# Performance work log

Hardware: AMD Instinct MI355X
Metric: run time of the kernel (lower is better)

The kernel has to match this reference:

```python
import jax, jax.numpy as jnp
import numpy as np

B, N, C, H, D = 1, 4096, 256, 8, 64  # batch, seq, channels, heads, head_dim


def setup_inputs() -> dict:
    key = jax.random.key(0)
    ks = jax.random.split(key, 11)
    s = 0.02
    return {
        "q_x": jax.random.normal(ks[0], (B, N, C), jnp.float32),
        "k_x": jax.random.normal(ks[1], (B, N, C), jnp.float32),
        "v_x": jax.random.normal(ks[2], (B, N, C), jnp.float32),
        "bias": jax.random.normal(ks[3], (B, 1, N, N), jnp.float32),
        "wq": jax.random.normal(ks[4], (H * D, C), jnp.float32) * s,
        "wk": jax.random.normal(ks[5], (H * D, C), jnp.float32) * s,
        "wv": jax.random.normal(ks[6], (H * D, C), jnp.float32) * s,
        "wg": jax.random.normal(ks[7], (H * D, C), jnp.float32) * s,
        "bg": jnp.ones((H * D,), jnp.float32),  # gating bias init = 1
        "wo": jax.random.normal(ks[8], (C, H * D), jnp.float32) * s,
        "bo": jnp.zeros((C,), jnp.float32),
        "q_chunk_size": 256,
        "kv_chunk_size": 1024,
    }


def reference(q_x, k_x, v_x, bias, wq, wk, wv, wg, bg, wo, bo,
              q_chunk_size, kv_chunk_size):
    # The chunked Rabe-Staats loop computes exact softmax attention; the
    # chunk sizes are memory knobs only, so the reference computes the
    # mathematically identical full attention.
    q = (q_x @ wq.T).reshape(*q_x.shape[:-1], H, D) / jnp.sqrt(jnp.asarray(D, q_x.dtype))
    k = (k_x @ wk.T).reshape(*k_x.shape[:-1], H, D)
    v = (v_x @ wv.T).reshape(*v_x.shape[:-1], H, D)
    logits = jnp.einsum("bqhd,bkhd->bhqk", q, k) + bias  # [B,H,Q,K]
    p = jax.nn.softmax(logits, axis=-1)
    o = jnp.einsum("bkhd,bhqk->bqhd", v, p)  # [B,Q,H,D]
    g = jax.nn.sigmoid(q_x @ wg.T + bg).reshape(*q_x.shape[:-1], H, D)
    o = o * g
    o = o.reshape(*o.shape[:-2], H * D)
    return o @ wo.T + bo
```

## Files before the change

### kernel.cpp

```cpp
#include <hip/hip_runtime.h>
#include <stdint.h>

#define NN 4096
#define CC 256
#define HD 512
#define DD 64
#define KSPLIT 2
#define KCHUNK (NN / KSPLIT)

typedef __attribute__((ext_vector_type(8))) short short8;
typedef __attribute__((ext_vector_type(4))) float floatx4;

__device__ __forceinline__ unsigned short f2bf(float x) {
    union { float f; unsigned int u; } v; v.f = x;
    unsigned int u = v.u + 0x7fffu + ((v.u >> 16) & 1u);
    return (unsigned short)(u >> 16);
}
__device__ __forceinline__ float bf2f(unsigned short s) {
    union { unsigned int u; float f; } v; v.u = ((unsigned int)s) << 16;
    return v.f;
}

__global__ __launch_bounds__(256) void proj_kernel(
    const float* __restrict__ qx, const float* __restrict__ kx,
    const float* __restrict__ vx,
    const float* __restrict__ wq, const float* __restrict__ wk,
    const float* __restrict__ wv, const float* __restrict__ wg,
    const float* __restrict__ bg,
    unsigned short* __restrict__ Qb, unsigned short* __restrict__ Kb,
    unsigned short* __restrict__ VbT, unsigned short* __restrict__ Gb)
{
    const int mode = blockIdx.z;
    const float* X = (mode == 1) ? kx : (mode == 2) ? vx : qx;
    const float* W = (mode == 0) ? wq : (mode == 1) ? wk : (mode == 2) ? wv : wg;

    const int m0 = blockIdx.x * 64;
    const int n0 = blockIdx.y * 64;
    const int tid = threadIdx.x;
    const int wid = tid >> 6;
    const int lane = tid & 63;
    const int quad = lane >> 4;
    const int ln = lane & 15;

    __shared__ __align__(16) unsigned short Xs[64 * 72];
    __shared__ __align__(16) unsigned short Ws[64 * 72];

    floatx4 acc[4] = {};

    for (int k0 = 0; k0 < CC; k0 += 64) {
        #pragma unroll
        for (int i = 0; i < 4; i++) {
            int idx = i * 256 + tid;
            int r = idx >> 4, c4 = idx & 15;
            float4 x4 = *(const float4*)&X[(size_t)(m0 + r) * CC + k0 + c4 * 4];
            ushort4 p;
            p.x = f2bf(x4.x); p.y = f2bf(x4.y); p.z = f2bf(x4.z); p.w = f2bf(x4.w);
            *(ushort4*)&Xs[r * 72 + c4 * 4] = p;
        }
        #pragma unroll
        for (int i = 0; i < 4; i++) {
            int idx = i * 256 + tid;
            int r = idx >> 4, c4 = idx & 15;
            float4 w4 = *(const float4*)&W[(size_t)(n0 + r) * CC + k0 + c4 * 4];
            ushort4 p;
            p.x = f2bf(w4.x); p.y = f2bf(w4.y); p.z = f2bf(w4.z); p.w = f2bf(w4.w);
            *(ushort4*)&Ws[r * 72 + c4 * 4] = p;
        }
        __syncthreads();

        #pragma unroll
        for (int ks = 0; ks < 64; ks += 32) {
            short8 a = *(const short8*)&Xs[(wid * 16 + ln) * 72 + ks + quad * 8];
            #pragma unroll
            for (int n = 0; n < 4; n++) {
                short8 b = *(const short8*)&Ws[(n * 16 + ln) * 72 + ks + quad * 8];
                acc[n] = __builtin_amdgcn_mfma_f32_16x16x32_bf16(a, b, acc[n], 0, 0, 0);
            }
        }
        __syncthreads();
    }

    if (mode == 2) {
        #pragma unroll
        for (int n = 0; n < 4; n++) {
            int cl = n * 16 + ln;
            #pragma unroll
            for (int r = 0; r < 4; r++) {
                int rl = wid * 16 + quad * 4 + r;
                Xs[cl * 72 + rl] = f2bf(acc[n][r]);
            }
        }
        __syncthreads();
        #pragma unroll
        for (int i = 0; i < 2; i++) {
            int idx = i * 256 + tid;
            int d = idx >> 3, m8 = idx & 7;
            short8 vv = *(const short8*)&Xs[d * 72 + m8 * 8];
            *(short8*)&VbT[(size_t)(n0 + d) * NN + m0 + m8 * 8] = vv;
        }
    } else {
        unsigned short* Out = (mode == 0) ? Qb : (mode == 1) ? Kb : Gb;
        #pragma unroll
        for (int n = 0; n < 4; n++) {
            int col = n0 + n * 16 + ln;
            float bgv = (mode == 3) ? bg[col] : 0.0f;
            #pragma unroll
            for (int r = 0; r < 4; r++) {
                int row = m0 + wid * 16 + quad * 4 + r;
                float v = acc[n][r];
                if (mode == 0)      v *= 0.125f;
                else if (mode == 3) v = 1.0f / (1.0f + __expf(-(v + bgv)));
                Out[(size_t)row * HD + col] = f2bf(v);
            }
        }
    }
}

__global__ __launch_bounds__(256) void attn_kernel(
    const unsigned short* __restrict__ Qb, const unsigned short* __restrict__ Kb,
    const unsigned short* __restrict__ VbT,
    const float* __restrict__ bias,
    float* __restrict__ Opart, float* __restrict__ Lpart)
{
    const int h = blockIdx.y;
    const int q0 = blockIdx.x * 64;
    const int sp = blockIdx.z;
    const int kbeg = sp * KCHUNK;
    const int tid = threadIdx.x;
    const int wid = tid >> 6;
    const int lane = tid & 63;
    const int quad = lane >> 4;
    const int ln = lane & 15;

    __shared__ __align__(16) unsigned short Qs[64 * 72];
    __shared__ __align__(16) unsigned short Ks[64 * 72];
    __shared__ __align__(16) unsigned short Vs[64 * 72];
    __shared__ __align__(16) unsigned short Ps[64 * 72];

    #pragma unroll
    for (int i = 0; i < 2; i++) {
        int idx = i * 256 + tid;
        int r = idx >> 3, c8 = idx & 7;
        short8 qv = *(const short8*)&Qb[(size_t)(q0 + r) * HD + h * DD + c8 * 8];
        *(short8*)&Qs[r * 72 + c8 * 8] = qv;
    }

    floatx4 O[4] = {};
    float lsum[4] = {0.0f, 0.0f, 0.0f, 0.0f};

    for (int k0 = kbeg; k0 < kbeg + KCHUNK; k0 += 64) {
        #pragma unroll
        for (int i = 0; i < 2; i++) {
            int idx = i * 256 + tid;
            int r = idx >> 3, c8 = idx & 7;
            short8 kv = *(const short8*)&Kb[(size_t)(k0 + r) * HD + h * DD + c8 * 8];
            *(short8*)&Ks[r * 72 + c8 * 8] = kv;
        }
        #pragma unroll
        for (int i = 0; i < 2; i++) {
            int idx = i * 256 + tid;
            int d = idx >> 3, c8 = idx & 7;
            short8 vv = *(const short8*)&VbT[(size_t)(h * DD + d) * NN + k0 + c8 * 8];
            *(short8*)&Vs[d * 72 + c8 * 8] = vv;
        }

        float bv[4][4];
        #pragma unroll
        for (int r = 0; r < 4; r++) {
            int grow = q0 + wid * 16 + quad * 4 + r;
            const float* brow = &bias[(size_t)grow * NN + k0];
            #pragma unroll
            for (int n = 0; n < 4; n++) bv[r][n] = brow[n * 16 + ln];
        }
        __syncthreads();

        floatx4 S[4] = {};
        #pragma unroll
        for (int ks = 0; ks < 64; ks += 32) {
            short8 a = *(const short8*)&Qs[(wid * 16 + ln) * 72 + ks + quad * 8];
            #pragma unroll
            for (int n = 0; n < 4; n++) {
                short8 b = *(const short8*)&Ks[(n * 16 + ln) * 72 + ks + quad * 8];
                S[n] = __builtin_amdgcn_mfma_f32_16x16x32_bf16(a, b, S[n], 0, 0, 0);
            }
        }

        #pragma unroll
        for (int r = 0; r < 4; r++) {
            #pragma unroll
            for (int n = 0; n < 4; n++) {
                float p = __expf(S[n][r] + bv[r][n]);
                lsum[r] += p;
                Ps[(wid * 16 + quad * 4 + r) * 72 + n * 16 + ln] = f2bf(p);
            }
        }

        #pragma unroll
        for (int ks = 0; ks < 64; ks += 32) {
            short8 a = *(const short8*)&Ps[(wid * 16 + ln) * 72 + ks + quad * 8];
            #pragma unroll
            for (int nd = 0; nd < 4; nd++) {
                short8 b = *(const short8*)&Vs[(nd * 16 + ln) * 72 + ks + quad * 8];
                O[nd] = __builtin_amdgcn_mfma_f32_16x16x32_bf16(a, b, O[nd], 0, 0, 0);
            }
        }
        __syncthreads();
    }

    #pragma unroll
    for (int r = 0; r < 4; r++) {
        #pragma unroll
        for (int off = 1; off < 16; off <<= 1)
            lsum[r] += __shfl_xor(lsum[r], off);
        int grow = q0 + wid * 16 + quad * 4 + r;
        size_t base = ((size_t)(sp * 8 + h) * NN + grow) * 64;
        #pragma unroll
        for (int nd = 0; nd < 4; nd++)
            Opart[base + nd * 16 + ln] = O[nd][r];
        if (ln == 0)
            Lpart[(size_t)(sp * 8 + h) * NN + grow] = lsum[r];
    }
}

__global__ __launch_bounds__(256) void combine_kernel(
    const float* __restrict__ Opart, const float* __restrict__ Lpart,
    const unsigned short* __restrict__ Gb, unsigned short* __restrict__ OGb)
{
    const int tid = threadIdx.x;
    const int d = tid & 63;
    const int flat = blockIdx.x * 4 + (tid >> 6);
    const int h = flat >> 12;
    const int q = flat & (NN - 1);

    float l0 = Lpart[(size_t)(0 * 8 + h) * NN + q];
    float l1 = Lpart[(size_t)(1 * 8 + h) * NN + q];
    float inv = 1.0f / (l0 + l1);

    size_t o0 = ((size_t)(0 * 8 + h) * NN + q) * 64 + d;
    size_t o1 = ((size_t)(1 * 8 + h) * NN + q) * 64 + d;
    float o = (Opart[o0] + Opart[o1]) * inv;

    int col = h * DD + d;
    float g = bf2f(Gb[(size_t)q * HD + col]);
    OGb[(size_t)q * HD + col] = f2bf(o * g);
}

__global__ __launch_bounds__(256) void outproj_kernel(
    const unsigned short* __restrict__ OGb, const float* __restrict__ wo,
    const float* __restrict__ bo, float* __restrict__ out)
{
    const int m0 = blockIdx.x * 64;
    const int n0 = blockIdx.y * 64;
    const int tid = threadIdx.x;
    const int wid = tid >> 6;
    const int lane = tid & 63;
    const int quad = lane >> 4;
    const int ln = lane & 15;

    __shared__ __align__(16) unsigned short Xs[64 * 72];
    __shared__ __align__(16) unsigned short Ws[64 * 72];

    floatx4 acc[4] = {};

    for (int k0 = 0; k0 < HD; k0 += 64) {
        #pragma unroll
        for (int i = 0; i < 2; i++) {
            int idx = i * 256 + tid;
            int r = idx >> 3, c8 = idx & 7;
            *(short8*)&Xs[r * 72 + c8 * 8] =
                *(const short8*)&OGb[(size_t)(m0 + r) * HD + k0 + c8 * 8];
        }
        #pragma unroll
        for (int i = 0; i < 4; i++) {
            int idx = i * 256 + tid;
            int r = idx >> 4, c4 = idx & 15;
            float4 w4 = *(const float4*)&wo[(size_t)(n0 + r) * HD + k0 + c4 * 4];
            ushort4 p;
            p.x = f2bf(w4.x); p.y = f2bf(w4.y); p.z = f2bf(w4.z); p.w = f2bf(w4.w);
            *(ushort4*)&Ws[r * 72 + c4 * 4] = p;
        }
        __syncthreads();

        #pragma unroll
        for (int ks = 0; ks < 64; ks += 32) {
            short8 a = *(const short8*)&Xs[(wid * 16 + ln) * 72 + ks + quad * 8];
            #pragma unroll
            for (int n = 0; n < 4; n++) {
                short8 b = *(const short8*)&Ws[(n * 16 + ln) * 72 + ks + quad * 8];
                acc[n] = __builtin_amdgcn_mfma_f32_16x16x32_bf16(a, b, acc[n], 0, 0, 0);
            }
        }
        __syncthreads();
    }

    #pragma unroll
    for (int n = 0; n < 4; n++) {
        int col = n0 + n * 16 + ln;
        float bov = bo[col];
        #pragma unroll
        for (int r = 0; r < 4; r++) {
            int row = m0 + wid * 16 + quad * 4 + r;
            out[(size_t)row * CC + col] = acc[n][r] + bov;
        }
    }
}

extern "C" void kernel_launch(void* const* d_in, const int* in_sizes, int n_in,
                              void* d_out, int out_size, void* d_ws, size_t ws_size,
                              hipStream_t stream) {
    const float* qx   = (const float*)d_in[0];
    const float* kx   = (const float*)d_in[1];
    const float* vx   = (const float*)d_in[2];
    const float* bias = (const float*)d_in[3];
    const float* wq   = (const float*)d_in[4];
    const float* wk   = (const float*)d_in[5];
    const float* wv   = (const float*)d_in[6];
    const float* wg   = (const float*)d_in[7];
    const float* bg   = (const float*)d_in[8];
    const float* wo   = (const float*)d_in[9];
    const float* bo   = (const float*)d_in[10];
    float* out = (float*)d_out;

    char* ws = (char*)d_ws;
    unsigned short* Qb  = (unsigned short*)(ws);
    unsigned short* Kb  = (unsigned short*)(ws + ((size_t)4  << 20));
    unsigned short* VbT = (unsigned short*)(ws + ((size_t)8  << 20));
    unsigned short* Gb  = (unsigned short*)(ws + ((size_t)12 << 20));
    unsigned short* OGb = (unsigned short*)(ws + ((size_t)16 << 20));
    float* Opart = (float*)(ws + ((size_t)20 << 20));
    float* Lpart = (float*)(ws + ((size_t)37 << 20));

    proj_kernel<<<dim3(64, 8, 4), 256, 0, stream>>>(
        qx, kx, vx, wq, wk, wv, wg, bg, Qb, Kb, VbT, Gb);
    attn_kernel<<<dim3(64, 8, KSPLIT), 256, 0, stream>>>(
        Qb, Kb, VbT, bias, Opart, Lpart);
    combine_kernel<<<dim3(NN * 8 / 4), 256, 0, stream>>>(
        Opart, Lpart, Gb, OGb);
    outproj_kernel<<<dim3(64, 4), 256, 0, stream>>>(
        OGb, wo, bo, out);
}
```

Baseline: 253.7 us.

## Pre-convert inputs to bf16, enlarge projection tiles, split K four ways

Adds a prep kernel that converts the activations and weights to bf16 once, folding the 1/sqrt(D) scale into wq. The projection GEMM moves to 128x128 tiles with a 2x2 warp grid, so each LDS fragment feeds more MFMAs. Attention keeps Q fragments in registers instead of staging them through LDS, raises KSPLIT from 2 to 4 for more blocks, and stores the partial outputs as bf16 to halve combine traffic. The costs are an extra launch, a workspace overlap between Opart and the bf16 input buffers, and reduced precision in the partial sums.

```diff
diff --git a/kernel.cpp b/kernel.cpp
--- a/kernel.cpp
+++ b/kernel.cpp
@@ -5,7 +5,7 @@
 #define CC 256
 #define HD 512
 #define DD 64
-#define KSPLIT 2
+#define KSPLIT 4
 #define KCHUNK (NN / KSPLIT)
 
 typedef __attribute__((ext_vector_type(8))) short short8;
@@ -21,97 +21,137 @@
     return v.f;
 }
 
-__global__ __launch_bounds__(256) void proj_kernel(
+__global__ __launch_bounds__(256) void prep_kernel(
     const float* __restrict__ qx, const float* __restrict__ kx,
     const float* __restrict__ vx,
     const float* __restrict__ wq, const float* __restrict__ wk,
     const float* __restrict__ wv, const float* __restrict__ wg,
+    const float* __restrict__ wo,
+    unsigned short* __restrict__ qxb, unsigned short* __restrict__ kxb,
+    unsigned short* __restrict__ vxb, unsigned short* __restrict__ Wb,
+    unsigned short* __restrict__ wob)
+{
+    const int z = blockIdx.y;
+    const float* src; unsigned short* dst; int n; float s = 1.0f;
+    switch (z) {
+        case 0: src = qx; dst = qxb; n = NN * CC; break;
+        case 1: src = kx; dst = kxb; n = NN * CC; break;
+        case 2: src = vx; dst = vxb; n = NN * CC; break;
+        case 3: src = wq; dst = Wb;              n = HD * CC; s = 0.125f; break;
+        case 4: src = wk; dst = Wb + 1 * HD * CC; n = HD * CC; break;
+        case 5: src = wv; dst = Wb + 2 * HD * CC; n = HD * CC; break;
+        case 6: src = wg; dst = Wb + 3 * HD * CC; n = HD * CC; break;
+        default: src = wo; dst = wob;            n = CC * HD; break;
+    }
+    int i = (blockIdx.x * 256 + threadIdx.x) * 4;
+    if (i < n) {
+        float4 v = *(const float4*)&src[i];
+        ushort4 p;
+        p.x = f2bf(v.x * s); p.y = f2bf(v.y * s);
+        p.z = f2bf(v.z * s); p.w = f2bf(v.w * s);
+        *(ushort4*)&dst[i] = p;
+    }
+}
+
+__global__ __launch_bounds__(256) void proj_kernel(
+    const unsigned short* __restrict__ qxb, const unsigned short* __restrict__ kxb,
+    const unsigned short* __restrict__ vxb, const unsigned short* __restrict__ Wb,
     const float* __restrict__ bg,
     unsigned short* __restrict__ Qb, unsigned short* __restrict__ Kb,
     unsigned short* __restrict__ VbT, unsigned short* __restrict__ Gb)
 {
-    const int mode = blockIdx.z;
-    const float* X = (mode == 1) ? kx : (mode == 2) ? vx : qx;
-    const float* W = (mode == 0) ? wq : (mode == 1) ? wk : (mode == 2) ? wv : wg;
-
-    const int m0 = blockIdx.x * 64;
-    const int n0 = blockIdx.y * 64;
+    const int m0 = blockIdx.x * 128;
+    const int nb = blockIdx.y;
+    const int n0 = nb * 128;
+    const int mode = nb >> 2;
+    const unsigned short* X = (mode == 1) ? kxb : (mode == 2) ? vxb : qxb;
+
     const int tid = threadIdx.x;
     const int wid = tid >> 6;
+    const int wr = wid >> 1, wc = wid & 1;
     const int lane = tid & 63;
     const int quad = lane >> 4;
     const int ln = lane & 15;
 
-    __shared__ __align__(16) unsigned short Xs[64 * 72];
-    __shared__ __align__(16) unsigned short Ws[64 * 72];
-
-    floatx4 acc[4] = {};
+    __shared__ __align__(16) unsigned short smem[2 * 128 * 72];
+    unsigned short* Xs = smem;
+    unsigned short* Ws = smem + 128 * 72;
+
+    floatx4 acc[4][4] = {};
 
     for (int k0 = 0; k0 < CC; k0 += 64) {
         #pragma unroll
         for (int i = 0; i < 4; i++) {
             int idx = i * 256 + tid;
-            int r = idx >> 4, c4 = idx & 15;
-            float4 x4 = *(const float4*)&X[(size_t)(m0 + r) * CC + k0 + c4 * 4];
-            ushort4 p;
-            p.x = f2bf(x4.x); p.y = f2bf(x4.y); p.z = f2bf(x4.z); p.w = f2bf(x4.w);
-            *(ushort4*)&Xs[r * 72 + c4 * 4] = p;
+            int r = idx >> 3, c8 = idx & 7;
+            *(short8*)&Xs[r * 72 + c8 * 8] =
+                *(const short8*)&X[(size_t)(m0 + r) * CC + k0 + c8 * 8];
         }
         #pragma unroll
         for (int i = 0; i < 4; i++) {
             int idx = i * 256 + tid;
-            int r = idx >> 4, c4 = idx & 15;
-            float4 w4 = *(const float4*)&W[(size_t)(n0 + r) * CC + k0 + c4 * 4];
-            ushort4 p;
-            p.x = f2bf(w4.x); p.y = f2bf(w4.y); p.z = f2bf(w4.z); p.w = f2bf(w4.w);
-            *(ushort4*)&Ws[r * 72 + c4 * 4] = p;
+            int r = idx >> 3, c8 = idx & 7;
+            *(short8*)&Ws[r * 72 + c8 * 8] =
+                *(const short8*)&Wb[(size_t)(n0 + r) * CC + k0 + c8 * 8];
         }
         __syncthreads();
 
         #pragma unroll
         for (int ks = 0; ks < 64; ks += 32) {
-            short8 a = *(const short8*)&Xs[(wid * 16 + ln) * 72 + ks + quad * 8];
-            #pragma unroll
-            for (int n = 0; n < 4; n++) {
-                short8 b = *(const short8*)&Ws[(n * 16 + ln) * 72 + ks + quad * 8];
-                acc[n] = __builtin_amdgcn_mfma_f32_16x16x32_bf16(a, b, acc[n], 0, 0, 0);
-            }
-        }
-        __syncthreads();
-    }
-
-    if (mode == 2) {
-        #pragma unroll
-        for (int n = 0; n < 4; n++) {
-            int cl = n * 16 + ln;
-            #pragma unroll
-            for (int r = 0; r < 4; r++) {
-                int rl = wid * 16 + quad * 4 + r;
-                Xs[cl * 72 + rl] = f2bf(acc[n][r]);
-            }
-        }
-        __syncthreads();
-        #pragma unroll
-        for (int i = 0; i < 2; i++) {
-            int idx = i * 256 + tid;
-            int d = idx >> 3, m8 = idx & 7;
-            short8 vv = *(const short8*)&Xs[d * 72 + m8 * 8];
-            *(short8*)&VbT[(size_t)(n0 + d) * NN + m0 + m8 * 8] = vv;
+            short8 a[4], b[4];
+            #pragma unroll
+            for (int i = 0; i < 4; i++)
+                a[i] = *(const short8*)&Xs[(wr * 64 + i * 16 + ln) * 72 + ks + quad * 8];
+            #pragma unroll
+            for (int j = 0; j < 4; j++)
+                b[j] = *(const short8*)&Ws[(wc * 64 + j * 16 + ln) * 72 + ks + quad * 8];
+            #pragma unroll
+            for (int i = 0; i < 4; i++)
+                #pragma unroll
+                for (int j = 0; j < 4; j++)
+                    acc[i][j] = __builtin_amdgcn_mfma_f32_16x16x32_bf16(a[i], b[j], acc[i][j], 0, 0, 0);
+        }
+        __syncthreads();
+    }
+
+    const int subn = nb & 3;
+    if (mode != 2) {
+        unsigned short* Out = (mode == 0) ? Qb : (mode == 1) ? Kb : Gb;
+        #pragma unroll
+        for (int i = 0; i < 4; i++) {
+            #pragma unroll
+            for (int j = 0; j < 4; j++) {
+                int col = subn * 128 + wc * 64 + j * 16 + ln;
+                float bgv = (mode == 3) ? bg[col] : 0.0f;
+                #pragma unroll
+                for (int r = 0; r < 4; r++) {
+                    int row = m0 + wr * 64 + i * 16 + quad * 4 + r;
+                    float v = acc[i][j][r];
+                    if (mode == 3) v = 1.0f / (1.0f + __expf(-(v + bgv)));
+                    Out[(size_t)row * HD + col] = f2bf(v);
+                }
+            }
         }
     } else {
-        unsigned short* Out = (mode == 0) ? Qb : (mode == 1) ? Kb : Gb;
-        #pragma unroll
-        for (int n = 0; n < 4; n++) {
-            int col = n0 + n * 16 + ln;
-            float bgv = (mode == 3) ? bg[col] : 0.0f;
-            #pragma unroll
-            for (int r = 0; r < 4; r++) {
-                int row = m0 + wid * 16 + quad * 4 + r;
-                float v = acc[n][r];
-                if (mode == 0)      v *= 0.125f;
-                else if (mode == 3) v = 1.0f / (1.0f + __expf(-(v + bgv)));
-                Out[(size_t)row * HD + col] = f2bf(v);
-            }
+        #pragma unroll
+        for (int i = 0; i < 4; i++) {
+            #pragma unroll
+            for (int j = 0; j < 4; j++) {
+                int cl = wc * 64 + j * 16 + ln;
+                #pragma unroll
+                for (int r = 0; r < 4; r++) {
+                    int rl = wr * 64 + i * 16 + quad * 4 + r;
+                    smem[cl * 136 + rl] = f2bf(acc[i][j][r]);
+                }
+            }
+        }
+        __syncthreads();
+        #pragma unroll
+        for (int it = 0; it < 8; it++) {
+            int idx = it * 256 + tid;
+            int c = idx >> 4, ch = idx & 15;
+            short8 vv = *(const short8*)&smem[c * 136 + ch * 8];
+            *(short8*)&VbT[(size_t)(subn * 128 + c) * NN + m0 + ch * 8] = vv;
         }
     }
 }
@@ -120,7 +160,7 @@
     const unsigned short* __restrict__ Qb, const unsigned short* __restrict__ Kb,
     const unsigned short* __restrict__ VbT,
     const float* __restrict__ bias,
-    float* __restrict__ Opart, float* __restrict__ Lpart)
+    unsigned short* __restrict__ Opart, float* __restrict__ Lpart)
 {
     const int h = blockIdx.y;
     const int q0 = blockIdx.x * 64;
@@ -132,18 +172,13 @@
     const int quad = lane >> 4;
     const int ln = lane & 15;
 
-    __shared__ __align__(16) unsigned short Qs[64 * 72];
     __shared__ __align__(16) unsigned short Ks[64 * 72];
     __shared__ __align__(16) unsigned short Vs[64 * 72];
     __shared__ __align__(16) unsigned short Ps[64 * 72];
 
-    #pragma unroll
-    for (int i = 0; i < 2; i++) {
-        int idx = i * 256 + tid;
-        int r = idx >> 3, c8 = idx & 7;
-        short8 qv = *(const short8*)&Qb[(size_t)(q0 + r) * HD + h * DD + c8 * 8];
-        *(short8*)&Qs[r * 72 + c8 * 8] = qv;
-    }
+    const int qrow = q0 + wid * 16 + ln;
+    short8 qa0 = *(const short8*)&Qb[(size_t)qrow * HD + h * DD + quad * 8];
+    short8 qa1 = *(const short8*)&Qb[(size_t)qrow * HD + h * DD + 32 + quad * 8];
 
     floatx4 O[4] = {};
     float lsum[4] = {0.0f, 0.0f, 0.0f, 0.0f};
@@ -153,22 +188,21 @@
         for (int i = 0; i < 2; i++) {
             int idx = i * 256 + tid;
             int r = idx >> 3, c8 = idx & 7;
-            short8 kv = *(const short8*)&Kb[(size_t)(k0 + r) * HD + h * DD + c8 * 8];
-            *(short8*)&Ks[r * 72 + c8 * 8] = kv;
+            *(short8*)&Ks[r * 72 + c8 * 8] =
+                *(const short8*)&Kb[(size_t)(k0 + r) * HD + h * DD + c8 * 8];
         }
         #pragma unroll
         for (int i = 0; i < 2; i++) {
             int idx = i * 256 + tid;
             int d = idx >> 3, c8 = idx & 7;
-            short8 vv = *(const short8*)&VbT[(size_t)(h * DD + d) * NN + k0 + c8 * 8];
-            *(short8*)&Vs[d * 72 + c8 * 8] = vv;
+            *(short8*)&Vs[d * 72 + c8 * 8] =
+                *(const short8*)&VbT[(size_t)(h * DD + d) * NN + k0 + c8 * 8];
         }
 
         float bv[4][4];
         #pragma unroll
         for (int r = 0; r < 4; r++) {
-            int grow = q0 + wid * 16 + quad * 4 + r;
-            const float* brow = &bias[(size_t)grow * NN + k0];
+            const float* brow = &bias[(size_t)(q0 + wid * 16 + quad * 4 + r) * NN + k0];
             #pragma unroll
             for (int n = 0; n < 4; n++) bv[r][n] = brow[n * 16 + ln];
         }
@@ -176,13 +210,11 @@
 
         floatx4 S[4] = {};
         #pragma unroll
-        for (int ks = 0; ks < 64; ks += 32) {
-            short8 a = *(const short8*)&Qs[(wid * 16 + ln) * 72 + ks + quad * 8];
-            #pragma unroll
-            for (int n = 0; n < 4; n++) {
-                short8 b = *(const short8*)&Ks[(n * 16 + ln) * 72 + ks + quad * 8];
-                S[n] = __builtin_amdgcn_mfma_f32_16x16x32_bf16(a, b, S[n], 0, 0, 0);
-            }
+        for (int n = 0; n < 4; n++) {
+            short8 b0 = *(const short8*)&Ks[(n * 16 + ln) * 72 + quad * 8];
+            S[n] = __builtin_amdgcn_mfma_f32_16x16x32_bf16(qa0, b0, S[n], 0, 0, 0);
+            short8 b1 = *(const short8*)&Ks[(n * 16 + ln) * 72 + 32 + quad * 8];
+            S[n] = __builtin_amdgcn_mfma_f32_16x16x32_bf16(qa1, b1, S[n], 0, 0, 0);
         }
 
         #pragma unroll
@@ -216,14 +248,14 @@
         size_t base = ((size_t)(sp * 8 + h) * NN + grow) * 64;
         #pragma unroll
         for (int nd = 0; nd < 4; nd++)
-            Opart[base + nd * 16 + ln] = O[nd][r];
+            Opart[base + nd * 16 + ln] = f2bf(O[nd][r]);
         if (ln == 0)
             Lpart[(size_t)(sp * 8 + h) * NN + grow] = lsum[r];
     }
 }
 
 __global__ __launch_bounds__(256) void combine_kernel(
-    const float* __restrict__ Opart, const float* __restrict__ Lpart,
+    const unsigned short* __restrict__ Opart, const float* __restrict__ Lpart,
     const unsigned short* __restrict__ Gb, unsigned short* __restrict__ OGb)
 {
     const int tid = threadIdx.x;
@@ -232,21 +264,21 @@
     const int h = flat >> 12;
     const int q = flat & (NN - 1);
 
-    float l0 = Lpart[(size_t)(0 * 8 + h) * NN + q];
-    float l1 = Lpart[(size_t)(1 * 8 + h) * NN + q];
-    float inv = 1.0f / (l0 + l1);
-
-    size_t o0 = ((size_t)(0 * 8 + h) * NN + q) * 64 + d;
-    size_t o1 = ((size_t)(1 * 8 + h) * NN + q) * 64 + d;
-    float o = (Opart[o0] + Opart[o1]) * inv;
-
+    float l = 0.0f, o = 0.0f;
+    #pragma unroll
+    for (int sp = 0; sp < KSPLIT; sp++) {
+        size_t idx = (size_t)(sp * 8 + h) * NN + q;
+        l += Lpart[idx];
+        o += bf2f(Opart[idx * 64 + d]);
+    }
+    float inv = 1.0f / l;
     int col = h * DD + d;
     float g = bf2f(Gb[(size_t)q * HD + col]);
-    OGb[(size_t)q * HD + col] = f2bf(o * g);
+    OGb[(size_t)q * HD + col] = f2bf(o * inv * g);
 }
 
 __global__ __launch_bounds__(256) void outproj_kernel(
-    const unsigned short* __restrict__ OGb, const float* __restrict__ wo,
+    const unsigned short* __restrict__ OGb, const unsigned short* __restrict__ wob,
     const float* __restrict__ bo, float* __restrict__ out)
 {
     const int m0 = blockIdx.x * 64;
@@ -271,13 +303,11 @@
                 *(const short8*)&OGb[(size_t)(m0 + r) * HD + k0 + c8 * 8];
         }
         #pragma unroll
-        for (int i = 0; i < 4; i++) {
-            int idx = i * 256 + tid;
-            int r = idx >> 4, c4 = idx & 15;
-            float4 w4 = *(const float4*)&wo[(size_t)(n0 + r) * HD + k0 + c4 * 4];
-            ushort4 p;
-            p.x = f2bf(w4.x); p.y = f2bf(w4.y); p.z = f2bf(w4.z); p.w = f2bf(w4.w);
-            *(ushort4*)&Ws[r * 72 + c4 * 4] = p;
+        for (int i = 0; i < 2; i++) {
+            int idx = i * 256 + tid;
+            int r = idx >> 3, c8 = idx & 7;
+            *(short8*)&Ws[r * 72 + c8 * 8] =
+                *(const short8*)&wob[(size_t)(n0 + r) * HD + k0 + c8 * 8];
         }
         __syncthreads();
 
@@ -322,20 +352,28 @@
     float* out = (float*)d_out;
 
     char* ws = (char*)d_ws;
-    unsigned short* Qb  = (unsigned short*)(ws);
-    unsigned short* Kb  = (unsigned short*)(ws + ((size_t)4  << 20));
-    unsigned short* VbT = (unsigned short*)(ws + ((size_t)8  << 20));
-    unsigned short* Gb  = (unsigned short*)(ws + ((size_t)12 << 20));
-    unsigned short* OGb = (unsigned short*)(ws + ((size_t)16 << 20));
-    float* Opart = (float*)(ws + ((size_t)20 << 20));
-    float* Lpart = (float*)(ws + ((size_t)37 << 20));
-
-    proj_kernel<<<dim3(64, 8, 4), 256, 0, stream>>>(
-        qx, kx, vx, wq, wk, wv, wg, bg, Qb, Kb, VbT, Gb);
+    const size_t MB = (size_t)1 << 20;
+    unsigned short* wob   = (unsigned short*)(ws);
+    float*          Lpart = (float*)(ws + MB / 4);
+    unsigned short* Qb    = (unsigned short*)(ws + 1 * MB);
+    unsigned short* Kb    = (unsigned short*)(ws + 5 * MB);
+    unsigned short* VbT   = (unsigned short*)(ws + 9 * MB);
+    unsigned short* Gb    = (unsigned short*)(ws + 13 * MB);
+    unsigned short* OGb   = (unsigned short*)(ws + 17 * MB);
+    unsigned short* qxb   = (unsigned short*)(ws + 21 * MB);
+    unsigned short* kxb   = (unsigned short*)(ws + 23 * MB);
+    unsigned short* vxb   = (unsigned short*)(ws + 25 * MB);
+    unsigned short* Wb    = (unsigned short*)(ws + 27 * MB);
+    unsigned short* Opart = (unsigned short*)(ws + 21 * MB);
+
+    prep_kernel<<<dim3(NN * CC / (256 * 4), 8), 256, 0, stream>>>(
+        qx, kx, vx, wq, wk, wv, wg, wo, qxb, kxb, vxb, Wb, wob);
+    proj_kernel<<<dim3(32, 16), 256, 0, stream>>>(
+        qxb, kxb, vxb, Wb, bg, Qb, Kb, VbT, Gb);
     attn_kernel<<<dim3(64, 8, KSPLIT), 256, 0, stream>>>(
         Qb, Kb, VbT, bias, Opart, Lpart);
     combine_kernel<<<dim3(NN * 8 / 4), 256, 0, stream>>>(
         Opart, Lpart, Gb, OGb);
     outproj_kernel<<<dim3(64, 4), 256, 0, stream>>>(
-        OGb, wo, bo, out);
-}
+        OGb, wob, bo, out);
+}
```

Result: faster. 231.5 us (-8.8%).
